# Performance work log

Measured on AMD Instinct MI355X. Metric: run time of the kernel, lower is better.

Reference implementation:

```python
import jax, jax.numpy as jnp
import numpy as np

B, N, C, H = 32, 577, 768, 12  # seq len = num_patches + 1 (cls token)
HD = C // H
SCALE = HD ** -0.5


def setup_inputs() -> dict:
    key = jax.random.key(0)
    k1, k2, k3, k4, k5 = jax.random.split(key, 5)
    x = jax.random.normal(k1, (B, N, C), dtype=jnp.float32)
    qkv_w = jax.random.normal(k2, (3 * C, C), dtype=jnp.float32) * (C ** -0.5)
    proj_w = jax.random.normal(k3, (C, C), dtype=jnp.float32) * (C ** -0.5)
    proj_b = jax.random.normal(k4, (C,), dtype=jnp.float32) * 0.02
    # learned additive distance-bias mask (nn.Parameter in the original)
    attn_mask = jax.random.normal(k5, (H, N, N), dtype=jnp.float32) * 0.02
    return {"x": x, "qkv_w": qkv_w, "proj_w": proj_w, "proj_b": proj_b,
            "attn_mask": attn_mask}


def reference(x, qkv_w, proj_w, proj_b, attn_mask):
    b, n, c = x.shape
    # fused QKV projection (no bias, qkv_bias=False)
    qkv = (x @ qkv_w.T).reshape(b, n, 3, H, HD)
    qkv = jnp.transpose(qkv, (2, 0, 3, 1, 4))  # [3, B, H, N, HD]
    q, k, v = qkv[0], qkv[1], qkv[2]
    # scaled dot-product scores + learned additive mask (broadcast over batch)
    attn = jnp.einsum('bhnd,bhmd->bhnm', q, k) * SCALE + attn_mask
    attn = jax.nn.softmax(attn, axis=-1)
    out = jnp.einsum('bhnm,bhmd->bhnd', attn, v)
    out = jnp.transpose(out, (0, 2, 1, 3)).reshape(b, n, c)
    return out @ proj_w.T + proj_b
```

## Files before the change

kernel.cpp:

```cpp
#include <hip/hip_runtime.h>
#include <stdint.h>
#include <stddef.h>

#define B_SZ 32
#define NQ 577
#define CDIM 768
#define NH 12
#define HDIM 64
#define MROWS (B_SZ * NQ)
#define KDIM CDIM
#define VT_STRIDE 640
#define MK_STRIDE 640
#define SCALE_F 0.125f

typedef __bf16 bf16x8 __attribute__((ext_vector_type(8)));
typedef float f32x4 __attribute__((ext_vector_type(4)));
typedef unsigned short u16x8 __attribute__((ext_vector_type(8)));
typedef unsigned short u16x4 __attribute__((ext_vector_type(4)));

__device__ __forceinline__ unsigned short f2bf(float f) {
    unsigned int u = __builtin_bit_cast(unsigned int, f);
    return (unsigned short)((u + 0x7fffu + ((u >> 16) & 1u)) >> 16);
}
__device__ __forceinline__ float bf2f(unsigned short u) {
    unsigned int v = ((unsigned int)u) << 16;
    return __builtin_bit_cast(float, v);
}

__device__ __forceinline__ f32x4 mfma16(bf16x8 a, bf16x8 b, f32x4 c) {
    return __builtin_amdgcn_mfma_f32_16x16x32_bf16(a, b, c, 0, 0, 0);
}

__device__ __forceinline__ void gll16(const void* g, void* l) {
    __builtin_amdgcn_global_load_lds(
        (const __attribute__((address_space(1))) void*)g,
        (__attribute__((address_space(3))) void*)l, 16, 0, 0);
}

__global__ __launch_bounds__(256) void cvt_bf16(
    const float* __restrict__ src, unsigned short* __restrict__ dst, int n8)
{
    int i = blockIdx.x * blockDim.x + threadIdx.x;
    int stride = gridDim.x * blockDim.x;
    for (; i < n8; i += stride) {
        const float* p = src + (size_t)i * 8;
        f32x4 v0 = *(const f32x4*)p;
        f32x4 v1 = *(const f32x4*)(p + 4);
        u16x8 u;
        u[0] = f2bf(v0[0]); u[1] = f2bf(v0[1]); u[2] = f2bf(v0[2]); u[3] = f2bf(v0[3]);
        u[4] = f2bf(v1[0]); u[5] = f2bf(v1[1]); u[6] = f2bf(v1[2]); u[7] = f2bf(v1[3]);
        *(u16x8*)(dst + (size_t)i * 8) = u;
    }
}

__global__ __launch_bounds__(256) void cvt_mask(
    const float* __restrict__ src, unsigned short* __restrict__ dst)
{
    const int CH = MK_STRIDE / 8;
    int i = blockIdx.x * blockDim.x + threadIdx.x;
    int total = NH * NQ * CH;
    if (i >= total) return;
    int row = i / CH, c8 = (i % CH) * 8;
    const float* s = src + (size_t)row * NQ;
    u16x8 u;
#pragma unroll
    for (int j = 0; j < 8; ++j) {
        int c = c8 + j;
        u[j] = (c < NQ) ? f2bf(s[c]) : (unsigned short)0;
    }
    *(u16x8*)(dst + (size_t)row * MK_STRIDE + c8) = u;
}

#define GEMM_MAINLOOP(A_PTR, B_PTR, MCLAMP)                                        \
    const int tid = threadIdx.x;                                                   \
    const int wv = tid >> 6, lane = tid & 63;                                      \
    const int lo = lane & 15, hi = lane >> 4;                                      \
    const int wr = wv >> 1, wc = wv & 1;                                           \
    f32x4 acc[4][4];                                                               \
    _Pragma("unroll") for (int i = 0; i < 4; ++i)                                  \
        _Pragma("unroll") for (int j = 0; j < 4; ++j)                              \
            acc[i][j] = (f32x4){0.f, 0.f, 0.f, 0.f};                               \
    const int c0 = wv * 128 + lane;                                                \
    const int c1 = c0 + 64;                                                        \
    const int rA0 = c0 >> 2, kA0 = (c0 & 3) * 8;                                   \
    const int rA1 = c1 >> 2, kA1 = (c1 & 3) * 8;                                   \
    int gra0 = mt * 128 + rA0; if (MCLAMP && gra0 >= MROWS) gra0 = MROWS - 1;      \
    int gra1 = mt * 128 + rA1; if (MCLAMP && gra1 >= MROWS) gra1 = MROWS - 1;      \
    const int grb0 = nt * 128 + rA0, grb1 = nt * 128 + rA1;                        \
    unsigned short* As_d0 = As + (size_t)c0 * 8;                                   \
    unsigned short* As_d1 = As + (size_t)c1 * 8;                                   \
    unsigned short* Bs_d0 = Bs + (size_t)c0 * 8;                                   \
    unsigned short* Bs_d1 = Bs + (size_t)c1 * 8;                                   \
    for (int k0 = 0; k0 < KDIM; k0 += 32) {                                        \
        gll16(A_PTR + (size_t)gra0 * KDIM + k0 + kA0, As_d0);                      \
        gll16(A_PTR + (size_t)gra1 * KDIM + k0 + kA1, As_d1);                      \
        gll16(B_PTR + (size_t)grb0 * KDIM + k0 + kA0, Bs_d0);                      \
        gll16(B_PTR + (size_t)grb1 * KDIM + k0 + kA1, Bs_d1);                      \
        __syncthreads();                                                           \
        bf16x8 af[4], bfr[4];                                                      \
        _Pragma("unroll") for (int mi = 0; mi < 4; ++mi)                           \
            af[mi] = *(const bf16x8*)(As + (wr * 64 + mi * 16 + lo) * 32 + hi * 8);\
        _Pragma("unroll") for (int nj = 0; nj < 4; ++nj)                           \
            bfr[nj] = *(const bf16x8*)(Bs + (wc * 64 + nj * 16 + lo) * 32 + hi * 8);\
        _Pragma("unroll") for (int mi = 0; mi < 4; ++mi)                           \
            _Pragma("unroll") for (int nj = 0; nj < 4; ++nj)                       \
                acc[mi][nj] = mfma16(af[mi], bfr[nj], acc[mi][nj]);                \
        __syncthreads();                                                           \
    }

__global__ __launch_bounds__(256) void qkv_gemm(
    const unsigned short* __restrict__ A,
    const unsigned short* __restrict__ Bm,
    unsigned short* __restrict__ qb,
    unsigned short* __restrict__ kb,
    unsigned short* __restrict__ vtb)
{
    __shared__ unsigned short As[128 * 32];
    __shared__ unsigned short Bs[128 * 32];
    const int NT = 18;
    int nt = blockIdx.x % NT, mt = blockIdx.x / NT;

    GEMM_MAINLOOP(A, Bm, 1)

    const int s = nt / 6;
    const int h = (nt % 6) * 2 + wc;
#pragma unroll
    for (int mi = 0; mi < 4; ++mi) {
#pragma unroll
        for (int r = 0; r < 4; ++r) {
            int m = mt * 128 + wr * 64 + mi * 16 + hi * 4 + r;
            if (m >= MROWS) continue;
            int b = m / NQ, n = m % NQ;
            size_t bh = (size_t)(b * NH + h);
#pragma unroll
            for (int nj = 0; nj < 4; ++nj) {
                int d = nj * 16 + lo;
                unsigned short bv = f2bf(acc[mi][nj][r]);
                if (s == 0)      qb[(bh * NQ + n) * HDIM + d] = bv;
                else if (s == 1) kb[(bh * NQ + n) * HDIM + d] = bv;
                else             vtb[(bh * HDIM + d) * VT_STRIDE + n] = bv;
            }
        }
    }
}

__global__ __launch_bounds__(256) void proj_gemm(
    const unsigned short* __restrict__ A,
    const unsigned short* __restrict__ Bm,
    const float* __restrict__ bias,
    float* __restrict__ out)
{
    __shared__ unsigned short As[128 * 32];
    __shared__ unsigned short Bs[128 * 32];
    const int NT = 6;
    int nt = blockIdx.x % NT, mt = blockIdx.x / NT;

    GEMM_MAINLOOP(A, Bm, 1)

    float bv[4];
#pragma unroll
    for (int nj = 0; nj < 4; ++nj) bv[nj] = bias[nt * 128 + wc * 64 + nj * 16 + lo];
#pragma unroll
    for (int mi = 0; mi < 4; ++mi)
#pragma unroll
        for (int r = 0; r < 4; ++r) {
            int m = mt * 128 + wr * 64 + mi * 16 + hi * 4 + r;
            if (m >= MROWS) continue;
#pragma unroll
            for (int nj = 0; nj < 4; ++nj)
                out[(size_t)m * CDIM + nt * 128 + wc * 64 + nj * 16 + lo] =
                    acc[mi][nj][r] + bv[nj];
        }
}


#define STAGE(SEL, KV)                                                        \
    {                                                                         \
        int kr0 = (KV) + srow;      if (kr0 > NQ - 1) kr0 = NQ - 1;           \
        int kr1 = (KV) + srow + 32; if (kr1 > NQ - 1) kr1 = NQ - 1;           \
        gll16(kp + (size_t)kr0 * HDIM + scol, &Ks[SEL][0] + tid * 8);         \
        gll16(kp + (size_t)kr1 * HDIM + scol, &Ks[SEL][2048] + tid * 8);      \
        gll16(vp + (size_t)srow * VT_STRIDE + (KV) + scol, &Vs[SEL][0] + tid * 8); \
        gll16(vp + (size_t)(srow + 32) * VT_STRIDE + (KV) + scol, &Vs[SEL][2048] + tid * 8); \
    }

#define LOADM(MW, KV)                                                         \
    _Pragma("unroll") for (int nj = 0; nj < 4; ++nj)                          \
        MW[nj] = *(const u16x4*)(mrow + (KV) + 16 * nj + 4 * hi);

#define ATTN_COMPUTE(CB, KV)                                                  \
    {                                                                         \
        const int kv0 = (KV);                                                 \
        bf16x8 af0[4], af1[4], bv0[4], bv1[4];                                \
        _Pragma("unroll") for (int nj = 0; nj < 4; ++nj) {                    \
            int kr = 16 * nj + lo;                                            \
            int sw = (kr & 7) << 4;                                           \
            const unsigned short* rowp = &Ks[CB][kr * 64];                    \
            af0[nj] = *(const bf16x8*)(rowp + ((( 0 + 16 * hi) ^ sw) >> 1));  \
            af1[nj] = *(const bf16x8*)(rowp + (((64 + 16 * hi) ^ sw) >> 1));  \
        }                                                                     \
        _Pragma("unroll") for (int dj = 0; dj < 4; ++dj) {                    \
            int dr = 16 * dj + lo;                                            \
            int sw = (dr & 7) << 4;                                           \
            const unsigned short* rowp = &Vs[CB][dr * 64];                    \
            bv0[dj] = *(const bf16x8*)(rowp + ((( 0 + 16 * hi) ^ sw) >> 1));  \
            bv1[dj] = *(const bf16x8*)(rowp + (((64 + 16 * hi) ^ sw) >> 1));  \
        }                                                                     \
        __builtin_amdgcn_s_setprio(1);                                        \
        f32x4 S[4];                                                           \
        _Pragma("unroll") for (int nj = 0; nj < 4; ++nj) {                    \
            f32x4 sv = (f32x4){0.f, 0.f, 0.f, 0.f};                           \
            sv = mfma16(af0[nj], bq0, sv);                                    \
            sv = mfma16(af1[nj], bq1, sv);                                    \
            S[nj] = sv;                                                       \
        }                                                                     \
        __builtin_amdgcn_s_setprio(0);                                        \
        float p[16];                                                          \
        _Pragma("unroll") for (int nj = 0; nj < 4; ++nj)                      \
            _Pragma("unroll") for (int r = 0; r < 4; ++r)                     \
                p[nj * 4 + r] = S[nj][r] * SCALE_F + bf2f(mw[nj][r]);         \
        if (kv0 + 64 > NQ) {                                                  \
            const int rem = NQ - kv0;                                         \
            _Pragma("unroll") for (int nj = 0; nj < 4; ++nj)                  \
                _Pragma("unroll") for (int r = 0; r < 4; ++r)                 \
                    if (16 * nj + 4 * hi + r >= rem) p[nj * 4 + r] = -1e30f;  \
        }                                                                     \
        float m01 = fmaxf(p[0], p[1]),  m23 = fmaxf(p[2], p[3]);              \
        float m45 = fmaxf(p[4], p[5]),  m67 = fmaxf(p[6], p[7]);              \
        float m89 = fmaxf(p[8], p[9]),  mab = fmaxf(p[10], p[11]);            \
        float mcd = fmaxf(p[12], p[13]), mef = fmaxf(p[14], p[15]);           \
        float pmax = fmaxf(fmaxf(fmaxf(m01, m23), fmaxf(m45, m67)),           \
                           fmaxf(fmaxf(m89, mab), fmaxf(mcd, mef)));          \
        pmax = fmaxf(pmax, __shfl_xor(pmax, 16));                             \
        pmax = fmaxf(pmax, __shfl_xor(pmax, 32));                             \
        bool grow = pmax > m_run + 8.f;                                       \
        float mnew = grow ? pmax : m_run;                                     \
        float corr = __expf(m_run - mnew);                                    \
        m_run = mnew;                                                         \
        if (__any((int)grow)) {                                               \
            float c0 = __shfl(corr, 4 * hi + 0);                              \
            float c1 = __shfl(corr, 4 * hi + 1);                              \
            float c2 = __shfl(corr, 4 * hi + 2);                              \
            float c3 = __shfl(corr, 4 * hi + 3);                              \
            _Pragma("unroll") for (int dj = 0; dj < 4; ++dj) {                \
                accO[dj][0] *= c0; accO[dj][1] *= c1;                         \
                accO[dj][2] *= c2; accO[dj][3] *= c3;                         \
            }                                                                 \
        }                                                                     \
        _Pragma("unroll") for (int i = 0; i < 16; ++i)                        \
            p[i] = __expf(p[i] - mnew);                                       \
        float ps = (((p[0]+p[1])+(p[2]+p[3])) + ((p[4]+p[5])+(p[6]+p[7])))    \
                 + (((p[8]+p[9])+(p[10]+p[11])) + ((p[12]+p[13])+(p[14]+p[15])));\
        _Pragma("unroll") for (int nj = 0; nj < 4; ++nj) {                    \
            u16x4 w;                                                          \
            w[0] = f2bf(p[nj*4+0]); w[1] = f2bf(p[nj*4+1]);                   \
            w[2] = f2bf(p[nj*4+2]); w[3] = f2bf(p[nj*4+3]);                   \
            *(u16x4*)&P_lds[wv][lo][16 * nj + 4 * hi] = w;                    \
        }                                                                     \
        ps += __shfl_xor(ps, 16);                                             \
        ps += __shfl_xor(ps, 32);                                             \
        l_run = l_run * corr + ps;                                            \
        const bf16x8 pa0 = *(const bf16x8*)&P_lds[wv][lo][8 * hi];            \
        const bf16x8 pa1 = *(const bf16x8*)&P_lds[wv][lo][32 + 8 * hi];       \
        __builtin_amdgcn_s_setprio(1);                                        \
        _Pragma("unroll") for (int dj = 0; dj < 4; ++dj) {                    \
            accO[dj] = mfma16(pa0, bv0[dj], accO[dj]);                        \
            accO[dj] = mfma16(pa1, bv1[dj], accO[dj]);                        \
        }                                                                     \
        __builtin_amdgcn_s_setprio(0);                                        \
    }

__global__ __launch_bounds__(256) void attn_fused(
    const unsigned short* __restrict__ qb,
    const unsigned short* __restrict__ kb,
    const unsigned short* __restrict__ vtb,
    const unsigned short* __restrict__ maskb,
    unsigned short* __restrict__ ob)
{
    __shared__ unsigned short Ks[2][64 * 64];
    __shared__ unsigned short Vs[2][64 * 64];
    __shared__ unsigned short P_lds[4][16][68];
    const int tid = threadIdx.x;
    const int wv = tid >> 6;
    const int lane = tid & 63;
    const int lo = lane & 15, hi = lane >> 4;

    const int xcd = blockIdx.x & 7;
    const int idx = blockIdx.x >> 3;
    const int bh = xcd + 8 * (idx / 10);
    const int qblk = idx % 10;
    const int b = bh / NH, h = bh % NH;
    const int qt0 = qblk * 64;

    const unsigned short* qp = qb + (size_t)bh * NQ * HDIM;
    const unsigned short* kp = kb + (size_t)bh * NQ * HDIM;
    const unsigned short* vp = vtb + (size_t)bh * HDIM * VT_STRIDE;

    const int srow = tid >> 3;
    const int scol = ((((tid & 7) << 4) ^ ((srow & 7) << 4)) >> 1);

    int qr = qt0 + 16 * wv + lo; if (qr > NQ - 1) qr = NQ - 1;
    const unsigned short* mrow = maskb + ((size_t)h * NQ + qr) * MK_STRIDE;
    const bf16x8 bq0 = *(const bf16x8*)(qp + (size_t)qr * HDIM + 8 * hi);
    const bf16x8 bq1 = *(const bf16x8*)(qp + (size_t)qr * HDIM + 32 + 8 * hi);

    float m_run = -1e30f, l_run = 0.f;
    f32x4 accO[4];
#pragma unroll
    for (int dj = 0; dj < 4; ++dj) accO[dj] = (f32x4){0.f, 0.f, 0.f, 0.f};

    u16x4 mw[4];
    STAGE(0, 0)
    for (int t = 0; t < 9; ++t) {
        const int kv0 = t * 64;
        LOADM(mw, kv0)
        asm volatile("" ::: "memory");
        STAGE((t + 1) & 1, kv0 + 64)
        asm volatile("s_waitcnt vmcnt(8)" ::: "memory");
        __builtin_amdgcn_s_barrier();
        asm volatile("" ::: "memory");
        ATTN_COMPUTE(t & 1, kv0)
        asm volatile("" ::: "memory");
        __builtin_amdgcn_s_barrier();
    }
    LOADM(mw, 576)
    asm volatile("s_waitcnt vmcnt(4)" ::: "memory");
    __builtin_amdgcn_s_barrier();
    asm volatile("" ::: "memory");
    ATTN_COMPUTE(1, 576)

    float linv[4];
#pragma unroll
    for (int r = 0; r < 4; ++r) linv[r] = 1.0f / __shfl(l_run, 4 * hi + r);
#pragma unroll
    for (int r = 0; r < 4; ++r) {
        int row = qt0 + 16 * wv + 4 * hi + r;
        if (row >= NQ) continue;
        size_t base = ((size_t)b * NQ + row) * CDIM + h * HDIM;
#pragma unroll
        for (int dj = 0; dj < 4; ++dj)
            ob[base + dj * 16 + lo] = f2bf(accO[dj][r] * linv[r]);
    }
}

extern "C" void kernel_launch(void* const* d_in, const int* in_sizes, int n_in,
                              void* d_out, int out_size, void* d_ws, size_t ws_size,
                              hipStream_t stream) {
    (void)in_sizes; (void)n_in; (void)out_size; (void)ws_size;
    const float* x      = (const float*)d_in[0];
    const float* qkv_w  = (const float*)d_in[1];
    const float* proj_w = (const float*)d_in[2];
    const float* proj_b = (const float*)d_in[3];
    const float* mask   = (const float*)d_in[4];
    float* out = (float*)d_out;

    const size_t x_elems  = (size_t)MROWS * CDIM;
    const size_t w_elems  = (size_t)3 * CDIM * CDIM;
    const size_t pw_elems = (size_t)CDIM * CDIM;
    const size_t mk_elems = (size_t)NH * NQ * MK_STRIDE;
    const size_t qk_elems = (size_t)B_SZ * NH * NQ * HDIM;
    const size_t vt_elems = (size_t)B_SZ * NH * HDIM * VT_STRIDE;

    unsigned short* xb    = (unsigned short*)d_ws;
    unsigned short* wb    = xb + x_elems;
    unsigned short* pwb   = wb + w_elems;
    unsigned short* mkb   = pwb + pw_elems;
    unsigned short* vtbuf = mkb + mk_elems;
    unsigned short* qbuf  = vtbuf + vt_elems;
    unsigned short* kbuf  = qbuf + qk_elems;
    unsigned short* aobuf = xb;

    cvt_bf16<<<1024, 256, 0, stream>>>(x, xb, (int)(x_elems / 8));
    cvt_bf16<<<256, 256, 0, stream>>>(qkv_w, wb, (int)(w_elems / 8));
    cvt_bf16<<<128, 256, 0, stream>>>(proj_w, pwb, (int)(pw_elems / 8));
    cvt_mask<<<(NH * NQ * (MK_STRIDE / 8) + 255) / 256, 256, 0, stream>>>(mask, mkb);
    qkv_gemm<<<145 * 18, 256, 0, stream>>>(xb, wb, qbuf, kbuf, vtbuf);
    attn_fused<<<12 * 32 * 10, 256, 0, stream>>>(qbuf, kbuf, vtbuf, mkb, aobuf);
    proj_gemm<<<145 * 6, 256, 0, stream>>>(aobuf, pwb, proj_b, out);
}
```

Baseline: 323.2 us.

## Double-buffer GEMM LDS tiles and remap workgroups across XCDs

The QKV and projection GEMM main loop now uses two LDS buffers, so the global-to-LDS loads for the next K slice are issued before computing on the current one. The loop keeps one barrier per iteration instead of two. Block IDs are also remapped so that each XCD gets a contiguous range of tiles, which is meant to improve L2 reuse of the shared A and B rows. This doubles the GEMM LDS footprint, which may reduce occupancy.

After: 321.4 us. Within noise of the previous version (-0.6%).

```diff
diff --git a/kernel.cpp b/kernel.cpp
--- a/kernel.cpp
+++ b/kernel.cpp
@@ -87,21 +87,25 @@
     int gra0 = mt * 128 + rA0; if (MCLAMP && gra0 >= MROWS) gra0 = MROWS - 1;      \
     int gra1 = mt * 128 + rA1; if (MCLAMP && gra1 >= MROWS) gra1 = MROWS - 1;      \
     const int grb0 = nt * 128 + rA0, grb1 = nt * 128 + rA1;                        \
-    unsigned short* As_d0 = As + (size_t)c0 * 8;                                   \
-    unsigned short* As_d1 = As + (size_t)c1 * 8;                                   \
-    unsigned short* Bs_d0 = Bs + (size_t)c0 * 8;                                   \
-    unsigned short* Bs_d1 = Bs + (size_t)c1 * 8;                                   \
-    for (int k0 = 0; k0 < KDIM; k0 += 32) {                                        \
-        gll16(A_PTR + (size_t)gra0 * KDIM + k0 + kA0, As_d0);                      \
-        gll16(A_PTR + (size_t)gra1 * KDIM + k0 + kA1, As_d1);                      \
-        gll16(B_PTR + (size_t)grb0 * KDIM + k0 + kA0, Bs_d0);                      \
-        gll16(B_PTR + (size_t)grb1 * KDIM + k0 + kA1, Bs_d1);                      \
-        __syncthreads();                                                           \
+    gll16(A_PTR + (size_t)gra0 * KDIM + kA0, &As[0][c0 * 8]);                      \
+    gll16(A_PTR + (size_t)gra1 * KDIM + kA1, &As[0][c1 * 8]);                      \
+    gll16(B_PTR + (size_t)grb0 * KDIM + kA0, &Bs[0][c0 * 8]);                      \
+    gll16(B_PTR + (size_t)grb1 * KDIM + kA1, &Bs[0][c1 * 8]);                      \
+    __syncthreads();                                                               \
+    for (int ks = 0; ks < KDIM / 32; ++ks) {                                       \
+        const int cur = ks & 1, nxt = cur ^ 1;                                     \
+        if (ks + 1 < KDIM / 32) {                                                  \
+            const int k0n = (ks + 1) * 32;                                         \
+            gll16(A_PTR + (size_t)gra0 * KDIM + k0n + kA0, &As[nxt][c0 * 8]);      \
+            gll16(A_PTR + (size_t)gra1 * KDIM + k0n + kA1, &As[nxt][c1 * 8]);      \
+            gll16(B_PTR + (size_t)grb0 * KDIM + k0n + kA0, &Bs[nxt][c0 * 8]);      \
+            gll16(B_PTR + (size_t)grb1 * KDIM + k0n + kA1, &Bs[nxt][c1 * 8]);      \
+        }                                                                          \
         bf16x8 af[4], bfr[4];                                                      \
         _Pragma("unroll") for (int mi = 0; mi < 4; ++mi)                           \
-            af[mi] = *(const bf16x8*)(As + (wr * 64 + mi * 16 + lo) * 32 + hi * 8);\
+            af[mi] = *(const bf16x8*)(&As[cur][(wr * 64 + mi * 16 + lo) * 32 + hi * 8]); \
         _Pragma("unroll") for (int nj = 0; nj < 4; ++nj)                           \
-            bfr[nj] = *(const bf16x8*)(Bs + (wc * 64 + nj * 16 + lo) * 32 + hi * 8);\
+            bfr[nj] = *(const bf16x8*)(&Bs[cur][(wc * 64 + nj * 16 + lo) * 32 + hi * 8]); \
         _Pragma("unroll") for (int mi = 0; mi < 4; ++mi)                           \
             _Pragma("unroll") for (int nj = 0; nj < 4; ++nj)                       \
                 acc[mi][nj] = mfma16(af[mi], bfr[nj], acc[mi][nj]);                \
@@ -115,10 +119,13 @@
     unsigned short* __restrict__ kb,
     unsigned short* __restrict__ vtb)
 {
-    __shared__ unsigned short As[128 * 32];
-    __shared__ unsigned short Bs[128 * 32];
+    __shared__ unsigned short As[2][128 * 32];
+    __shared__ unsigned short Bs[2][128 * 32];
     const int NT = 18;
-    int nt = blockIdx.x % NT, mt = blockIdx.x / NT;
+    const int q8 = 326, r8 = 2;
+    const int xcd = blockIdx.x & 7, off = blockIdx.x >> 3;
+    const int wgid = (xcd < r8 ? xcd * (q8 + 1) : r8 * (q8 + 1) + (xcd - r8) * q8) + off;
+    int nt = wgid % NT, mt = wgid / NT;
 
     GEMM_MAINLOOP(A, Bm, 1)
 
@@ -150,10 +157,13 @@
     const float* __restrict__ bias,
     float* __restrict__ out)
 {
-    __shared__ unsigned short As[128 * 32];
-    __shared__ unsigned short Bs[128 * 32];
+    __shared__ unsigned short As[2][128 * 32];
+    __shared__ unsigned short Bs[2][128 * 32];
     const int NT = 6;
-    int nt = blockIdx.x % NT, mt = blockIdx.x / NT;
+    const int q8 = 108, r8 = 6;
+    const int xcd = blockIdx.x & 7, off = blockIdx.x >> 3;
+    const int wgid = (xcd < r8 ? xcd * (q8 + 1) : r8 * (q8 + 1) + (xcd - r8) * q8) + off;
+    int nt = wgid % NT, mt = wgid / NT;
 
     GEMM_MAINLOOP(A, Bm, 1)
 
@@ -172,7 +182,6 @@
                     acc[mi][nj][r] + bv[nj];
         }
 }
-
 
 #define STAGE(SEL, KV)                                                        \
     {                                                                         \
```

## Rewrite QKV and projection GEMMs with 256x256 tiles and pipelined LDS staging

Applied to the files above, without the earlier changes.

Both GEMMs move from 128x128 tiles with 256 threads and a synchronous load-then-compute loop to 256x256 tiles with 512 threads (8 waves). Global-to-LDS loads run through a double-buffered, multi-stage prefetch with swizzled LDS layout, and MFMA phases are interleaved with explicit barriers and s_setprio. Workgroup IDs are remapped so neighbouring tiles land on the same XCD. The intent is more data reuse per tile, fewer LDS bank conflicts, and hiding memory latency; the cost is much larger LDS and register use, and with only 657 and 219 blocks the grid may fill the GPU poorly.

Result: faster. 311.6 us (-3.6%).

```diff
diff --git a/kernel.cpp b/kernel.cpp
--- a/kernel.cpp
+++ b/kernel.cpp
@@ -9,6 +9,7 @@
 #define HDIM 64
 #define MROWS (B_SZ * NQ)
 #define KDIM CDIM
+#define NKT (KDIM / 64)
 #define VT_STRIDE 640
 #define MK_STRIDE 640
 #define SCALE_F 0.125f
@@ -71,64 +72,135 @@
     *(u16x8*)(dst + (size_t)row * MK_STRIDE + c8) = u;
 }
 
-#define GEMM_MAINLOOP(A_PTR, B_PTR, MCLAMP)                                        \
+
+#define STAGE_HT8(SC, A_PTR, B_PTR)                                                \
+    { const int _t = (SC) >> 2, _p = (SC) & 3;                                     \
+      if (_t < NKT) {                                                              \
+        const int _kh = _p >> 1;                                                   \
+        unsigned short* _dst = (_p & 1) ? &Bl[_t & 1][_kh][0] : &Al[_t & 1][_kh][0];\
+        const unsigned short* _sb = (_p & 1) ? (B_PTR) : (A_PTR);                  \
+        const int _rb = ((_p & 1) ? nt : mt) * 256;                                \
+        const int _k = _t * 64 + _kh * 32;                                         \
+        const int _c0 = tid, _c1 = tid + 512;                                      \
+        const int _g0 = _c0 ^ ((_c0 >> 3) & 7), _g1 = _c1 ^ ((_c1 >> 3) & 7);      \
+        int _r0 = _rb + (_g0 >> 2), _r1 = _rb + (_g1 >> 2);                        \
+        if (!(_p & 1)) {                                                           \
+            if (_r0 >= MROWS) _r0 = MROWS - 1;                                     \
+            if (_r1 >= MROWS) _r1 = MROWS - 1;                                     \
+        }                                                                          \
+        gll16(_sb + (size_t)_r0 * KDIM + _k + (_g0 & 3) * 8, _dst + _c0 * 8);      \
+        gll16(_sb + (size_t)_r1 * KDIM + _k + (_g1 & 3) * 8, _dst + _c1 * 8);      \
+      } else {                                                                     \
+        gll16(A_PTR, &Scr[tid * 8]);                                               \
+        gll16(A_PTR, &Scr[(tid + 512) * 8]);                                       \
+      } }
+
+#define GEMM8_MAINLOOP(A_PTR, B_PTR)                                               \
     const int tid = threadIdx.x;                                                   \
-    const int wv = tid >> 6, lane = tid & 63;                                      \
+    const int wid = tid >> 6, lane = tid & 63;                                     \
     const int lo = lane & 15, hi = lane >> 4;                                      \
-    const int wr = wv >> 1, wc = wv & 1;                                           \
-    f32x4 acc[4][4];                                                               \
-    _Pragma("unroll") for (int i = 0; i < 4; ++i)                                  \
+    const int wr = wid >> 2, wcN = wid & 3;                                        \
+    f32x4 acc[8][4];                                                               \
+    _Pragma("unroll") for (int i = 0; i < 8; ++i)                                  \
         _Pragma("unroll") for (int j = 0; j < 4; ++j)                              \
             acc[i][j] = (f32x4){0.f, 0.f, 0.f, 0.f};                               \
-    const int c0 = wv * 128 + lane;                                                \
-    const int c1 = c0 + 64;                                                        \
-    const int rA0 = c0 >> 2, kA0 = (c0 & 3) * 8;                                   \
-    const int rA1 = c1 >> 2, kA1 = (c1 & 3) * 8;                                   \
-    int gra0 = mt * 128 + rA0; if (MCLAMP && gra0 >= MROWS) gra0 = MROWS - 1;      \
-    int gra1 = mt * 128 + rA1; if (MCLAMP && gra1 >= MROWS) gra1 = MROWS - 1;      \
-    const int grb0 = nt * 128 + rA0, grb1 = nt * 128 + rA1;                        \
-    unsigned short* As_d0 = As + (size_t)c0 * 8;                                   \
-    unsigned short* As_d1 = As + (size_t)c1 * 8;                                   \
-    unsigned short* Bs_d0 = Bs + (size_t)c0 * 8;                                   \
-    unsigned short* Bs_d1 = Bs + (size_t)c1 * 8;                                   \
-    for (int k0 = 0; k0 < KDIM; k0 += 32) {                                        \
-        gll16(A_PTR + (size_t)gra0 * KDIM + k0 + kA0, As_d0);                      \
-        gll16(A_PTR + (size_t)gra1 * KDIM + k0 + kA1, As_d1);                      \
-        gll16(B_PTR + (size_t)grb0 * KDIM + k0 + kA0, Bs_d0);                      \
-        gll16(B_PTR + (size_t)grb1 * KDIM + k0 + kA1, Bs_d1);                      \
-        __syncthreads();                                                           \
-        bf16x8 af[4], bfr[4];                                                      \
-        _Pragma("unroll") for (int mi = 0; mi < 4; ++mi)                           \
-            af[mi] = *(const bf16x8*)(As + (wr * 64 + mi * 16 + lo) * 32 + hi * 8);\
-        _Pragma("unroll") for (int nj = 0; nj < 4; ++nj)                           \
-            bfr[nj] = *(const bf16x8*)(Bs + (wc * 64 + nj * 16 + lo) * 32 + hi * 8);\
-        _Pragma("unroll") for (int mi = 0; mi < 4; ++mi)                           \
-            _Pragma("unroll") for (int nj = 0; nj < 4; ++nj)                       \
-                acc[mi][nj] = mfma16(af[mi], bfr[nj], acc[mi][nj]);                \
-        __syncthreads();                                                           \
-    }
-
-__global__ __launch_bounds__(256) void qkv_gemm(
+    const int xsw = ((4 * lo + hi) ^ ((lo >> 1) & 7)) * 16;                        \
+    _Pragma("unroll") for (int ps = 0; ps < 7; ++ps) { STAGE_HT8(ps, A_PTR, B_PTR) } \
+    int sc = 7;                                                                    \
+    asm volatile("s_waitcnt vmcnt(6)" ::: "memory");                               \
+    __builtin_amdgcn_s_barrier();                                                  \
+    for (int t = 0; t < NKT; ++t) {                                                \
+        const int db = t & 1;                                                      \
+        const char* a0p = (const char*)&Al[db][0][0] + xsw;                        \
+        const char* a1p = (const char*)&Al[db][1][0] + xsw;                        \
+        const char* b0p = (const char*)&Bl[db][0][0] + xsw;                        \
+        const char* b1p = (const char*)&Bl[db][1][0] + xsw;                        \
+        bf16x8 a[8], bx[2], by[2];                                                 \
+              \
+        _Pragma("unroll") for (int mi = 0; mi < 8; ++mi)                           \
+            a[mi] = *(const bf16x8*)(a0p + (wr * 8 + mi) * 1024);                  \
+        bx[0] = *(const bf16x8*)(b0p + (wcN * 4 + 0) * 1024);                      \
+        bx[1] = *(const bf16x8*)(b0p + (wcN * 4 + 1) * 1024);                      \
+        asm volatile("" ::: "memory");                                             \
+        STAGE_HT8(sc, A_PTR, B_PTR) ++sc;                                          \
+        __builtin_amdgcn_s_barrier();                                              \
+        __builtin_amdgcn_s_setprio(1);                                             \
+        _Pragma("unroll") for (int mi = 0; mi < 8; ++mi) {                         \
+            acc[mi][0] = mfma16(a[mi], bx[0], acc[mi][0]);                         \
+            acc[mi][1] = mfma16(a[mi], bx[1], acc[mi][1]);                         \
+        }                                                                          \
+        __builtin_amdgcn_s_setprio(0);                                             \
+        __builtin_amdgcn_s_barrier();                                              \
+                               \
+        by[0] = *(const bf16x8*)(b0p + (wcN * 4 + 2) * 1024);                      \
+        by[1] = *(const bf16x8*)(b0p + (wcN * 4 + 3) * 1024);                      \
+        asm volatile("" ::: "memory");                                             \
+        STAGE_HT8(sc, A_PTR, B_PTR) ++sc;                                          \
+        __builtin_amdgcn_s_barrier();                                              \
+        __builtin_amdgcn_s_setprio(1);                                             \
+        _Pragma("unroll") for (int mi = 0; mi < 8; ++mi) {                         \
+            acc[mi][2] = mfma16(a[mi], by[0], acc[mi][2]);                         \
+            acc[mi][3] = mfma16(a[mi], by[1], acc[mi][3]);                         \
+        }                                                                          \
+        __builtin_amdgcn_s_setprio(0);                                             \
+        __builtin_amdgcn_s_barrier();                                              \
+                    \
+        _Pragma("unroll") for (int mi = 0; mi < 8; ++mi)                           \
+            a[mi] = *(const bf16x8*)(a1p + (wr * 8 + mi) * 1024);                  \
+        bx[0] = *(const bf16x8*)(b1p + (wcN * 4 + 0) * 1024);                      \
+        bx[1] = *(const bf16x8*)(b1p + (wcN * 4 + 1) * 1024);                      \
+        asm volatile("" ::: "memory");                                             \
+        STAGE_HT8(sc, A_PTR, B_PTR) ++sc;                                          \
+        __builtin_amdgcn_s_barrier();                                              \
+        __builtin_amdgcn_s_setprio(1);                                             \
+        _Pragma("unroll") for (int mi = 0; mi < 8; ++mi) {                         \
+            acc[mi][0] = mfma16(a[mi], bx[0], acc[mi][0]);                         \
+            acc[mi][1] = mfma16(a[mi], bx[1], acc[mi][1]);                         \
+        }                                                                          \
+        __builtin_amdgcn_s_setprio(0);                                             \
+        __builtin_amdgcn_s_barrier();                                              \
+               \
+        by[0] = *(const bf16x8*)(b1p + (wcN * 4 + 2) * 1024);                      \
+        by[1] = *(const bf16x8*)(b1p + (wcN * 4 + 3) * 1024);                      \
+        asm volatile("" ::: "memory");                                             \
+        STAGE_HT8(sc, A_PTR, B_PTR) ++sc;                                          \
+        asm volatile("s_waitcnt vmcnt(6)" ::: "memory");                           \
+        __builtin_amdgcn_s_barrier();                                              \
+        __builtin_amdgcn_s_setprio(1);                                             \
+        _Pragma("unroll") for (int mi = 0; mi < 8; ++mi) {                         \
+            acc[mi][2] = mfma16(a[mi], by[0], acc[mi][2]);                         \
+            acc[mi][3] = mfma16(a[mi], by[1], acc[mi][3]);                         \
+        }                                                                          \
+        __builtin_amdgcn_s_setprio(0);                                             \
+        __builtin_amdgcn_s_barrier();                                              \
+    }                                                                              \
+    asm volatile("s_waitcnt vmcnt(0)" ::: "memory");
+
+__global__ __launch_bounds__(512, 2) void qkv_gemm(
     const unsigned short* __restrict__ A,
     const unsigned short* __restrict__ Bm,
     unsigned short* __restrict__ qb,
     unsigned short* __restrict__ kb,
     unsigned short* __restrict__ vtb)
 {
-    __shared__ unsigned short As[128 * 32];
-    __shared__ unsigned short Bs[128 * 32];
-    const int NT = 18;
-    int nt = blockIdx.x % NT, mt = blockIdx.x / NT;
-
-    GEMM_MAINLOOP(A, Bm, 1)
-
-    const int s = nt / 6;
-    const int h = (nt % 6) * 2 + wc;
-#pragma unroll
-    for (int mi = 0; mi < 4; ++mi) {
+    __shared__ __align__(16) unsigned short Al[2][2][256 * 32];
+    __shared__ __align__(16) unsigned short Bl[2][2][256 * 32];
+    __shared__ __align__(16) unsigned short Scr[512 * 16];
+    const int NTL = 9;
+    const int xcd = blockIdx.x & 7, off = blockIdx.x >> 3;
+    const int wgid = (xcd < 1 ? xcd * 83 : 83 + (xcd - 1) * 82) + off;
+    const int nt = wgid % NTL, mt = wgid / NTL;
+
+    GEMM8_MAINLOOP(A, Bm)
+
+    const int cbase = nt * 256 + wcN * 64;
+    const int s = cbase / CDIM;
+    const int h = (cbase % CDIM) / HDIM;
+#pragma unroll
+    for (int mi = 0; mi < 8; ++mi) {
 #pragma unroll
         for (int r = 0; r < 4; ++r) {
-            int m = mt * 128 + wr * 64 + mi * 16 + hi * 4 + r;
+            int m = mt * 256 + wr * 128 + mi * 16 + 4 * hi + r;
             if (m >= MROWS) continue;
             int b = m / NQ, n = m % NQ;
             size_t bh = (size_t)(b * NH + h);
@@ -144,35 +216,38 @@
     }
 }
 
-__global__ __launch_bounds__(256) void proj_gemm(
+__global__ __launch_bounds__(512, 2) void proj_gemm(
     const unsigned short* __restrict__ A,
     const unsigned short* __restrict__ Bm,
     const float* __restrict__ bias,
     float* __restrict__ out)
 {
-    __shared__ unsigned short As[128 * 32];
-    __shared__ unsigned short Bs[128 * 32];
-    const int NT = 6;
-    int nt = blockIdx.x % NT, mt = blockIdx.x / NT;
-
-    GEMM_MAINLOOP(A, Bm, 1)
-
+    __shared__ __align__(16) unsigned short Al[2][2][256 * 32];
+    __shared__ __align__(16) unsigned short Bl[2][2][256 * 32];
+    __shared__ __align__(16) unsigned short Scr[512 * 16];
+    const int NTL = 3;
+    const int xcd = blockIdx.x & 7, off = blockIdx.x >> 3;
+    const int wgid = (xcd < 3 ? xcd * 28 : 84 + (xcd - 3) * 27) + off;
+    const int nt = wgid % NTL, mt = wgid / NTL;
+
+    GEMM8_MAINLOOP(A, Bm)
+
+    const int cb = nt * 256 + wcN * 64;
     float bv[4];
 #pragma unroll
-    for (int nj = 0; nj < 4; ++nj) bv[nj] = bias[nt * 128 + wc * 64 + nj * 16 + lo];
-#pragma unroll
-    for (int mi = 0; mi < 4; ++mi)
+    for (int nj = 0; nj < 4; ++nj) bv[nj] = bias[cb + nj * 16 + lo];
+#pragma unroll
+    for (int mi = 0; mi < 8; ++mi) {
 #pragma unroll
         for (int r = 0; r < 4; ++r) {
-            int m = mt * 128 + wr * 64 + mi * 16 + hi * 4 + r;
+            int m = mt * 256 + wr * 128 + mi * 16 + 4 * hi + r;
             if (m >= MROWS) continue;
 #pragma unroll
             for (int nj = 0; nj < 4; ++nj)
-                out[(size_t)m * CDIM + nt * 128 + wc * 64 + nj * 16 + lo] =
-                    acc[mi][nj][r] + bv[nj];
+                out[(size_t)m * CDIM + cb + nj * 16 + lo] = acc[mi][nj][r] + bv[nj];
         }
-}
-
+    }
+}
 
 #define STAGE(SEL, KV)                                                        \
     {                                                                         \
@@ -374,7 +449,7 @@
     cvt_bf16<<<256, 256, 0, stream>>>(qkv_w, wb, (int)(w_elems / 8));
     cvt_bf16<<<128, 256, 0, stream>>>(proj_w, pwb, (int)(pw_elems / 8));
     cvt_mask<<<(NH * NQ * (MK_STRIDE / 8) + 255) / 256, 256, 0, stream>>>(mask, mkb);
-    qkv_gemm<<<145 * 18, 256, 0, stream>>>(xb, wb, qbuf, kbuf, vtbuf);
+    qkv_gemm<<<73 * 9, 512, 0, stream>>>(xb, wb, qbuf, kbuf, vtbuf);
     attn_fused<<<12 * 32 * 10, 256, 0, stream>>>(qbuf, kbuf, vtbuf, mkb, aobuf);
-    proj_gemm<<<145 * 6, 256, 0, stream>>>(aobuf, pwb, proj_b, out);
-}
+    proj_gemm<<<73 * 3, 512, 0, stream>>>(aobuf, pwb, proj_b, out);
+}
```
